# Performance work log

Measured on AMD Instinct MI355X. Metric: run time of the kernel, lower is better.

Reference implementation:

```python
import jax, jax.numpy as jnp
import numpy as np

T, B, H, SEQ = 64, 512, 512, 384


def setup_inputs() -> dict:
    key = jax.random.key(0)
    k1, k2 = jax.random.split(key)
    inputs = jax.random.normal(k1, (T, B, H), dtype=jnp.float32)
    initial_hidden = jax.random.uniform(k2, (H,), dtype=jnp.float32)
    # ops in {-1, 0, 1}; rewrite pops that would underflow pos below 0 to holds
    # (the original module has no protection, so valid usage keeps pos >= 0).
    rng = np.random.default_rng(0)
    ops_raw = rng.integers(-1, 2, size=(T, B))
    pos = np.zeros(B, dtype=np.int64)
    ops = np.empty((T, B), dtype=np.int32)
    for t in range(T):
        op = ops_raw[t]
        op = np.where(pos + op < 0, 0, op)
        pos = pos + op
        ops[t] = op
    return {
        "inputs": inputs,
        "initial_hidden": initial_hidden,
        "ops": jnp.asarray(ops),
        "seq_len": SEQ,
    }


def reference(inputs, initial_hidden, ops, seq_len):
    # inputs: (T, B, H) float; ops: (T, B) int32 in {-1,0,1}
    T_, B_, H_ = inputs.shape
    bidx = jnp.arange(B_)
    # build_stack: (seq_len+2, B, H), row 0 = initial_hidden broadcast, pos = 0
    stack0 = jnp.zeros((seq_len + 2, B_, H_), dtype=inputs.dtype)
    stack0 = stack0.at[0].set(jnp.broadcast_to(initial_hidden, (B_, H_)))
    pos0 = jnp.zeros((B_,), dtype=jnp.int32)

    def step(carry, xs):
        stack, pos = carry
        x, op = xs
        # scatter-write input at pos+1 per batch element
        stack = stack.at[pos + 1, bidx].set(x)
        # pos update
        pos = pos + op
        # gather-read at updated pos
        hidden = stack[pos, bidx]  # (B, H)
        return (stack, pos), hidden

    (_, _), hiddens = jax.lax.scan(step, (stack0, pos0), (inputs, ops))
    return hiddens  # (T, B, H)
```

## Files before the change

kernel.cpp:

```cpp
#include <hip/hip_runtime.h>

#define T_DIM 64
#define B_DIM 512
#define H_DIM 512
#define H4    (H_DIM / 4)

typedef float vfloat4 __attribute__((ext_vector_type(4)));

__global__ __launch_bounds__(256) void state_stack_fused(
        const vfloat4* __restrict__ in,
        const vfloat4* __restrict__ init,
        const int*     __restrict__ ops,
        vfloat4*       __restrict__ out) {
    const int b    = blockIdx.x >> 2;
    const int tq   = blockIdx.x & 3;
    const int wave = threadIdx.x >> 6;
    const int lane = threadIdx.x & 63;

    const int op = ops[lane * B_DIM + b];
    int pos = op;
#pragma unroll
    for (int d = 1; d < 64; d <<= 1) {
        int n = __shfl_up(pos, d, 64);
        if (lane >= d) pos += n;
    }
    const int w = pos - op + 1;

    __shared__ unsigned long long masks[4][65];
    masks[wave][lane] = 0ull;
    if (lane == 0) masks[wave][64] = 0ull;
    __builtin_amdgcn_wave_barrier();
    atomicOr(&masks[wave][w], 1ull << lane);
    __builtin_amdgcn_wave_barrier();
    unsigned long long m = masks[wave][pos];
    m &= (lane == 63) ? ~0ull : ((1ull << (lane + 1)) - 1ull);
    const int my_src = m ? (63 - __builtin_clzll(m)) : -1;

    const int t0 = tq * 16 + wave * 4;
#pragma unroll
    for (int r = 0; r < 4; ++r) {
        const int t = t0 + r;
        const int s = __shfl(my_src, t, 64);
        const vfloat4* src_row = (s < 0)
            ? init
            : in + ((size_t)(s * B_DIM + b)) * H4;
        const vfloat4 v0 = src_row[lane];
        const vfloat4 v1 = src_row[lane + 64];
        vfloat4* dst = out + ((size_t)(t * B_DIM + b)) * H4;
        __builtin_nontemporal_store(v0, dst + lane);
        __builtin_nontemporal_store(v1, dst + lane + 64);
    }
}

extern "C" void kernel_launch(void* const* d_in, const int* in_sizes, int n_in,
                              void* d_out, int out_size, void* d_ws, size_t ws_size,
                              hipStream_t stream) {
    const float* inputs = (const float*)d_in[0];
    const float* init   = (const float*)d_in[1];
    const int*   ops    = (const int*)d_in[2];

    state_stack_fused<<<B_DIM * 4, 256, 0, stream>>>(
        (const vfloat4*)inputs, (const vfloat4*)init, ops, (vfloat4*)d_out);
}
```

Measured before the change: 121.1 us.

## Swizzle block order, scalarize source index, and batch loads before stores

Remaps blockIdx so consecutive blocks are spread across XCDs and batch positions differently. The source row index is made wave-uniform with readfirstlane so the address computation can run on scalar registers. All four rows' loads are issued before any stores so more memory requests are in flight per wave. The cost is higher register pressure, and the swizzle changes L2 locality in ways that are hard to predict.

```diff
diff --git a/kernel.cpp b/kernel.cpp
--- a/kernel.cpp
+++ b/kernel.cpp
@@ -12,8 +12,9 @@
         const vfloat4* __restrict__ init,
         const int*     __restrict__ ops,
         vfloat4*       __restrict__ out) {
-    const int b    = blockIdx.x >> 2;
-    const int tq   = blockIdx.x & 3;
+    const unsigned swz = ((blockIdx.x & 7u) << 8) | (blockIdx.x >> 3);
+    const int b    = swz >> 2;
+    const int tq   = swz & 3;
     const int wave = threadIdx.x >> 6;
     const int lane = threadIdx.x & 63;
 
@@ -37,18 +38,26 @@
     const int my_src = m ? (63 - __builtin_clzll(m)) : -1;
 
     const int t0 = tq * 16 + wave * 4;
+
+    const vfloat4* srow[4];
 #pragma unroll
     for (int r = 0; r < 4; ++r) {
-        const int t = t0 + r;
-        const int s = __shfl(my_src, t, 64);
-        const vfloat4* src_row = (s < 0)
-            ? init
-            : in + ((size_t)(s * B_DIM + b)) * H4;
-        const vfloat4 v0 = src_row[lane];
-        const vfloat4 v1 = src_row[lane + 64];
-        vfloat4* dst = out + ((size_t)(t * B_DIM + b)) * H4;
-        __builtin_nontemporal_store(v0, dst + lane);
-        __builtin_nontemporal_store(v1, dst + lane + 64);
+        const int s = __builtin_amdgcn_readfirstlane(__shfl(my_src, t0 + r, 64));
+        srow[r] = (s < 0) ? init : in + ((size_t)(s * B_DIM + b)) * H4;
+    }
+
+    vfloat4 v0[4], v1[4];
+#pragma unroll
+    for (int r = 0; r < 4; ++r) {
+        v0[r] = srow[r][lane];
+        v1[r] = srow[r][lane + 64];
+    }
+
+#pragma unroll
+    for (int r = 0; r < 4; ++r) {
+        vfloat4* dst = out + ((size_t)((t0 + r) * B_DIM + b)) * H4;
+        __builtin_nontemporal_store(v0[r], dst + lane);
+        __builtin_nontemporal_store(v1[r], dst + lane + 64);
     }
 }
 
```

New measurement: 117.8 us (median of 2 runs). -2.7%, faster.
